# Performance work log

Measured on AMD Instinct MI355X. Metric: run time of the kernel, lower is better.

## Reference

```python
import jax, jax.numpy as jnp
import numpy as np

N_NODES = 50000
N_EDGES = 800000
D_IN, D_HID, D_OUT, D_EDGE = 128, 256, 128, 16


def setup_inputs() -> dict:
    key = jax.random.key(0)
    ks = jax.random.split(key, 6)
    nh = jax.random.normal(ks[0], (N_NODES, D_IN), dtype=jnp.float32)
    eh = jax.random.normal(ks[1], (N_EDGES, D_EDGE), dtype=jnp.float32)
    edge_index = jax.random.randint(ks[2], (2, N_EDGES), 0, N_NODES, dtype=jnp.int32)
    # MLP params (build_layer: Linear(d_in,d_hid) -> relu -> Linear(d_hid,d_out)), scaled init
    W1 = jax.random.normal(ks[3], (D_IN, D_HID), dtype=jnp.float32) / np.sqrt(D_IN)
    b1 = jnp.zeros((D_HID,), dtype=jnp.float32)
    W2 = jax.random.normal(ks[4], (D_HID, D_OUT), dtype=jnp.float32) / np.sqrt(D_HID)
    b2 = jnp.zeros((D_OUT,), dtype=jnp.float32)
    return {"nh": nh, "eh": eh, "edge_index": edge_index,
            "W1": W1, "b1": b1, "W2": W2, "b2": b2}


def reference(nh, eh, edge_index, W1, b1, W2, b2):
    n_nodes = nh.shape[0]
    # nf_lin: 2-layer MLP with relu
    n_h = jax.nn.relu(nh @ W1 + b1) @ W2 + b2          # [N, d]
    src, dst = edge_index[0], edge_index[1]
    src_nh = n_h[src]                                   # [E, d] gather
    dst_nh = n_h[dst]                                   # [E, d] gather
    attn = jnp.sum(src_nh * dst_nh, axis=-1)            # [E] per-edge score
    # segment softmax over edges grouped by destination node
    seg_max = jax.ops.segment_max(attn, dst, num_segments=n_nodes)  # [N]
    e = jnp.exp(attn - seg_max[dst])                    # [E] stable exp
    denom = jax.ops.segment_sum(e, dst, num_segments=n_nodes)       # [N]
    attn = e / denom[dst]                               # [E]
    # weighted scatter-add aggregation
    nz = jax.ops.segment_sum(attn[:, None] * src_nh, dst, num_segments=n_nodes)  # [N, d]
    return (n_h + nz, eh)
```

## Files before the change

kernel.cpp:

```cpp
#include <hip/hip_runtime.h>
#include <math.h>


#define D_IN   128
#define D_HID  256
#define D_OUT  128

typedef short bf16x8 __attribute__((ext_vector_type(8)));
typedef float f32x4  __attribute__((ext_vector_type(4)));

__device__ __forceinline__ short f2bf(float f)
{
    unsigned int u = __float_as_uint(f);
    unsigned int r = (u + 0x7fffu + ((u >> 16) & 1u)) >> 16;
    return (short)r;
}
__device__ __forceinline__ float bf2f(short h)
{
    return __uint_as_float(((unsigned int)(unsigned short)h) << 16);
}

__device__ __forceinline__ void pack_body(const float* __restrict__ W,
                                          short* __restrict__ Bh,
                                          short* __restrict__ Bl,
                                          int K, int N, int u)
{
    const int T = K >> 5;
    const int l = u & 63;
    const int t = (u >> 6) % T;
    const int c = u / (64 * T);
    const int lr = l & 15, kb = l >> 4;
    bf16x8 vh, vl;
#pragma unroll
    for (int j = 0; j < 8; ++j) {
        int k   = t * 32 + kb * 8 + j;
        int col = c * 16 + lr;
        float x = W[(size_t)k * N + col];
        short hi = f2bf(x);
        vh[j] = hi;
        vl[j] = f2bf(x - bf2f(hi));
    }
    *(bf16x8*)(Bh + (size_t)u * 8) = vh;
    *(bf16x8*)(Bl + (size_t)u * 8) = vl;
}

__global__ __launch_bounds__(256)
void prep(const float* __restrict__ A, short* __restrict__ Ah,
          short* __restrict__ Al, long valid, long total8, int nAB,
          const float* __restrict__ W1, short* __restrict__ B1h,
          short* __restrict__ B1l,
          const float* __restrict__ W2, short* __restrict__ B2h,
          short* __restrict__ B2l)
{
    int b = blockIdx.x;
    const int tid = threadIdx.x;
    if (b < nAB) {
        long t = (long)b * 256 + tid;
        if (t < total8) {
            long base = t * 8;
            bf16x8 vh, vl;
            if (base < valid) {
                float4 f0 = *(const float4*)(A + base);
                float4 f1 = *(const float4*)(A + base + 4);
                float fv[8] = {f0.x, f0.y, f0.z, f0.w, f1.x, f1.y, f1.z, f1.w};
#pragma unroll
                for (int j = 0; j < 8; ++j) {
                    short hi = f2bf(fv[j]);
                    vh[j] = hi;
                    vl[j] = f2bf(fv[j] - bf2f(hi));
                }
            } else {
                vh = (bf16x8)0; vl = (bf16x8)0;
            }
            *(bf16x8*)(Ah + base) = vh;
            *(bf16x8*)(Al + base) = vl;
        }
        return;
    }
    b -= nAB;
    if (b < 16) pack_body(W1, B1h, B1l, D_IN, D_HID, b * 256 + tid);
    else        pack_body(W2, B2h, B2l, D_HID, D_OUT, (b - 16) * 256 + tid);
}

__global__ __launch_bounds__(256)
void hist_pos(const int* __restrict__ dst, unsigned int* __restrict__ count,
              unsigned int* __restrict__ pos, int E)
{
    int e = blockIdx.x * blockDim.x + threadIdx.x;
    if (e < E) pos[e] = atomicAdd(count + dst[e], 1u);
}

__global__ __launch_bounds__(256)
void chunk_sums(const unsigned int* __restrict__ count,
                unsigned int* __restrict__ bsum, int n)
{
    __shared__ unsigned int lds[256];
    const int t = threadIdx.x;
    const int i = blockIdx.x * 256 + t;
    lds[t] = (i < n) ? count[i] : 0u;
    __syncthreads();
#pragma unroll
    for (int d = 128; d > 0; d >>= 1) {
        if (t < d) lds[t] += lds[t + d];
        __syncthreads();
    }
    if (t == 0) bsum[blockIdx.x] = lds[0];
}

__global__ __launch_bounds__(256)
void scan_sums(const unsigned int* __restrict__ bsum,
               unsigned int* __restrict__ boff, int nb)
{
    __shared__ unsigned int lds[256];
    const int t = threadIdx.x;
    unsigned int v = (t < nb) ? bsum[t] : 0u;
    lds[t] = v;
    __syncthreads();
#pragma unroll
    for (int d = 1; d < 256; d <<= 1) {
        unsigned int x = lds[t];
        unsigned int add = (t >= d) ? lds[t - d] : 0u;
        __syncthreads();
        lds[t] = x + add;
        __syncthreads();
    }
    if (t < nb) boff[t] = lds[t] - v;
}

__global__ __launch_bounds__(256)
void write_off(const unsigned int* __restrict__ count,
               const unsigned int* __restrict__ boff,
               unsigned int* __restrict__ off, int n)
{
    __shared__ unsigned int lds[256];
    const int t = threadIdx.x;
    const int i = blockIdx.x * 256 + t;
    unsigned int v = (i < n) ? count[i] : 0u;
    lds[t] = v;
    __syncthreads();
#pragma unroll
    for (int d = 1; d < 256; d <<= 1) {
        unsigned int x = lds[t];
        unsigned int add = (t >= d) ? lds[t - d] : 0u;
        __syncthreads();
        lds[t] = x + add;
        __syncthreads();
    }
    unsigned int incl = lds[t];
    unsigned int base = boff[blockIdx.x];
    if (i < n)  off[i] = base + incl - v;
    if (i == n - 1) off[n] = base + incl;
}

__global__ __launch_bounds__(256)
void fill_srcs(const int* __restrict__ src, const int* __restrict__ dst,
               const unsigned int* __restrict__ off,
               const unsigned int* __restrict__ pos,
               int* __restrict__ srcs, int E)
{
    int e = blockIdx.x * blockDim.x + threadIdx.x;
    if (e >= E) return;
    srcs[off[dst[e]] + pos[e]] = src[e];
}

#define H2_STRIDE 264

__global__ __launch_bounds__(256)
void mlp_fused(const short* __restrict__ Ah, const short* __restrict__ Al,
               const short* __restrict__ B1h, const short* __restrict__ B1l,
               const float* __restrict__ b1,
               const short* __restrict__ B2h, const short* __restrict__ B2l,
               const float* __restrict__ b2,
               float* __restrict__ out, short* __restrict__ nhb, int Nvalid)
{
    __shared__ __attribute__((aligned(16))) short H[64 * H2_STRIDE];

    const int w  = threadIdx.x >> 6;
    const int l  = threadIdx.x & 63;
    const int lr = l & 15, kb = l >> 4;
    const size_t row0 = (size_t)blockIdx.x * 64;

    f32x4 acc1[4][4] = {};
#pragma unroll
    for (int t = 0; t < 4; ++t) {
        bf16x8 ah[4], al[4], bh[4], bl[4];
#pragma unroll
        for (int m = 0; m < 4; ++m) {
            size_t aoff = (row0 + m * 16 + lr) * D_IN + t * 32 + kb * 8;
            ah[m] = *(const bf16x8*)(Ah + aoff);
            al[m] = *(const bf16x8*)(Al + aoff);
        }
#pragma unroll
        for (int n = 0; n < 4; ++n) {
            int c = w * 4 + n;
            size_t boff = (size_t)((c * 4 + t) * 64 + l) * 8;
            bh[n] = *(const bf16x8*)(B1h + boff);
            bl[n] = *(const bf16x8*)(B1l + boff);
        }
#pragma unroll
        for (int m = 0; m < 4; ++m)
#pragma unroll
            for (int n = 0; n < 4; ++n) {
                acc1[m][n] = __builtin_amdgcn_mfma_f32_16x16x32_bf16(ah[m], bh[n], acc1[m][n], 0, 0, 0);
                acc1[m][n] = __builtin_amdgcn_mfma_f32_16x16x32_bf16(al[m], bh[n], acc1[m][n], 0, 0, 0);
                acc1[m][n] = __builtin_amdgcn_mfma_f32_16x16x32_bf16(ah[m], bl[n], acc1[m][n], 0, 0, 0);
            }
    }

#pragma unroll
    for (int n = 0; n < 4; ++n) {
        int col = w * 64 + n * 16 + lr;
        float bb = b1[col];
#pragma unroll
        for (int m = 0; m < 4; ++m)
#pragma unroll
            for (int i = 0; i < 4; ++i) {
                int lrow = m * 16 + kb * 4 + i;
                float v = fmaxf(acc1[m][n][i] + bb, 0.f);
                H[lrow * H2_STRIDE + col] = f2bf(v);
            }
    }
    __syncthreads();

    f32x4 acc2[4][2] = {};
#pragma unroll
    for (int t2 = 0; t2 < 8; ++t2) {
        bf16x8 a[4], bh[2], bl[2];
#pragma unroll
        for (int m = 0; m < 4; ++m)
            a[m] = *(const bf16x8*)&H[(m * 16 + lr) * H2_STRIDE + t2 * 32 + kb * 8];
#pragma unroll
        for (int n = 0; n < 2; ++n) {
            int c = w * 2 + n;
            size_t boff = (size_t)((c * 8 + t2) * 64 + l) * 8;
            bh[n] = *(const bf16x8*)(B2h + boff);
            bl[n] = *(const bf16x8*)(B2l + boff);
        }
#pragma unroll
        for (int m = 0; m < 4; ++m)
#pragma unroll
            for (int n = 0; n < 2; ++n) {
                acc2[m][n] = __builtin_amdgcn_mfma_f32_16x16x32_bf16(a[m], bh[n], acc2[m][n], 0, 0, 0);
                acc2[m][n] = __builtin_amdgcn_mfma_f32_16x16x32_bf16(a[m], bl[n], acc2[m][n], 0, 0, 0);
            }
    }

#pragma unroll
    for (int n = 0; n < 2; ++n) {
        int col = w * 32 + n * 16 + lr;
        float bb = b2[col];
#pragma unroll
        for (int m = 0; m < 4; ++m)
#pragma unroll
            for (int i = 0; i < 4; ++i) {
                size_t row = row0 + m * 16 + kb * 4 + i;
                float v = acc2[m][n][i] + bb;
                nhb[row * D_OUT + col] = f2bf(v);
                if ((int)row < Nvalid) out[row * D_OUT + col] = v;
            }
    }
}

#define NEG_HUGE -3.0e38f

__global__ __launch_bounds__(256)
void agg_copy(const short* __restrict__ nhb,
              const unsigned int* __restrict__ off,
              const int* __restrict__ srcs,
              float* __restrict__ out, int N,
              const f32x4* __restrict__ ehin, f32x4* __restrict__ ehout,
              int n4, int copyB)
{
    if ((int)blockIdx.x < copyB) {
        for (int i = blockIdx.x * 256 + threadIdx.x; i < n4; i += copyB * 256) {
            f32x4 v = __builtin_nontemporal_load(ehin + i);
            __builtin_nontemporal_store(v, ehout + i);
        }
        return;
    }
    int wid  = (((int)blockIdx.x - copyB) * 256 + (int)threadIdx.x) >> 6;
    int lane = threadIdx.x & 63;
    if (wid >= N) return;
    const int g = lane >> 4;
    const int j = lane & 15;

    const float* sp = out + (size_t)wid * D_OUT + j * 8;
    const float4 sa = *(const float4*)sp;
    const float4 sb = *(const float4*)(sp + 4);

    const unsigned int beg = off[wid];
    const unsigned int end = off[wid + 1];

    float m = NEG_HUGE, den = 0.f;
    float c0 = 0.f, c1 = 0.f, c2 = 0.f, c3 = 0.f;
    float c4 = 0.f, c5 = 0.f, c6 = 0.f, c7 = 0.f;

    for (unsigned int base = beg; base < end; base += 8) {
        unsigned int idx0 = base + g * 2;
        unsigned int idx1 = idx0 + 1;
        bool v0 = idx0 < end, v1 = idx1 < end;
        int s0 = v0 ? srcs[idx0] : 0;
        int s1 = v1 ? srcs[idx1] : 0;
        uint4 A0 = *(const uint4*)(nhb + (size_t)s0 * D_OUT + j * 8);
        uint4 A1 = *(const uint4*)(nhb + (size_t)s1 * D_OUT + j * 8);

        float a00 = __uint_as_float(A0.x << 16), a01 = __uint_as_float(A0.x & 0xffff0000u);
        float a02 = __uint_as_float(A0.y << 16), a03 = __uint_as_float(A0.y & 0xffff0000u);
        float a04 = __uint_as_float(A0.z << 16), a05 = __uint_as_float(A0.z & 0xffff0000u);
        float a06 = __uint_as_float(A0.w << 16), a07 = __uint_as_float(A0.w & 0xffff0000u);
        float a10 = __uint_as_float(A1.x << 16), a11 = __uint_as_float(A1.x & 0xffff0000u);
        float a12 = __uint_as_float(A1.y << 16), a13 = __uint_as_float(A1.y & 0xffff0000u);
        float a14 = __uint_as_float(A1.z << 16), a15 = __uint_as_float(A1.z & 0xffff0000u);
        float a16 = __uint_as_float(A1.w << 16), a17 = __uint_as_float(A1.w & 0xffff0000u);

        float p0 = a00 * sa.x + a01 * sa.y + a02 * sa.z + a03 * sa.w
                 + a04 * sb.x + a05 * sb.y + a06 * sb.z + a07 * sb.w;
        float p1 = a10 * sa.x + a11 * sa.y + a12 * sa.z + a13 * sa.w
                 + a14 * sb.x + a15 * sb.y + a16 * sb.z + a17 * sb.w;
        p0 += __shfl_xor(p0, 1);  p1 += __shfl_xor(p1, 1);
        p0 += __shfl_xor(p0, 2);  p1 += __shfl_xor(p1, 2);
        p0 += __shfl_xor(p0, 4);  p1 += __shfl_xor(p1, 4);
        p0 += __shfl_xor(p0, 8);  p1 += __shfl_xor(p1, 8);

        float p0v = v0 ? p0 : NEG_HUGE;
        float p1v = v1 ? p1 : NEG_HUGE;
        float mnew = fmaxf(m, fmaxf(p0v, p1v));
        float scale = __expf(m - mnew);
        float w0 = v0 ? __expf(p0 - mnew) : 0.f;
        float w1 = v1 ? __expf(p1 - mnew) : 0.f;
        den = fmaf(den, scale, w0 + w1);
        c0 = fmaf(c0, scale, fmaf(w0, a00, w1 * a10));
        c1 = fmaf(c1, scale, fmaf(w0, a01, w1 * a11));
        c2 = fmaf(c2, scale, fmaf(w0, a02, w1 * a12));
        c3 = fmaf(c3, scale, fmaf(w0, a03, w1 * a13));
        c4 = fmaf(c4, scale, fmaf(w0, a04, w1 * a14));
        c5 = fmaf(c5, scale, fmaf(w0, a05, w1 * a15));
        c6 = fmaf(c6, scale, fmaf(w0, a06, w1 * a16));
        c7 = fmaf(c7, scale, fmaf(w0, a07, w1 * a17));
        m = mnew;
    }

    {
        float mg = m;
        m = fmaxf(m, __shfl_xor(m, 16));
        m = fmaxf(m, __shfl_xor(m, 32));
        float gs = __expf(mg - m);
        den *= gs;
        c0 *= gs; c1 *= gs; c2 *= gs; c3 *= gs;
        c4 *= gs; c5 *= gs; c6 *= gs; c7 *= gs;
#pragma unroll
        for (int o = 16; o < 64; o <<= 1) {
            den += __shfl_xor(den, o);
            c0 += __shfl_xor(c0, o); c1 += __shfl_xor(c1, o);
            c2 += __shfl_xor(c2, o); c3 += __shfl_xor(c3, o);
            c4 += __shfl_xor(c4, o); c5 += __shfl_xor(c5, o);
            c6 += __shfl_xor(c6, o); c7 += __shfl_xor(c7, o);
        }
    }

    float inv = (den > 0.f) ? 1.f / den : 0.f;
    if (g == 0) {
        float4 o0, o1;
        o0.x = sa.x + c0 * inv; o0.y = sa.y + c1 * inv;
        o0.z = sa.z + c2 * inv; o0.w = sa.w + c3 * inv;
        o1.x = sb.x + c4 * inv; o1.y = sb.y + c5 * inv;
        o1.z = sb.z + c6 * inv; o1.w = sb.w + c7 * inv;
        float* op = out + (size_t)wid * D_OUT + j * 8;
        *(float4*)op = o0;
        *(float4*)(op + 4) = o1;
    }
}

extern "C" void kernel_launch(void* const* d_in, const int* in_sizes, int n_in,
                              void* d_out, int out_size, void* d_ws, size_t ws_size,
                              hipStream_t stream)
{
    const float* nh  = (const float*)d_in[0];
    const float* eh  = (const float*)d_in[1];
    const int*   ei  = (const int*)d_in[2];
    const float* W1  = (const float*)d_in[3];
    const float* b1  = (const float*)d_in[4];
    const float* W2  = (const float*)d_in[5];
    const float* b2  = (const float*)d_in[6];

    const int N  = in_sizes[0] / D_IN;
    const int E  = in_sizes[2] / 2;
    const int EH = in_sizes[1];
    const int Mp = (N + 63) & ~63;
    const int NB = (N + 255) / 256;

    const int* src = ei;
    const int* dst = ei + E;

    float* out_nh = (float*)d_out;
    float* out_eh = (float*)d_out + (size_t)N * D_OUT;

    char* ws = (char*)d_ws;
    size_t o = 0;
    short* Ahp = (short*)(ws + o); o += (size_t)Mp * D_IN * 2;
    short* Alp = (short*)(ws + o); o += (size_t)Mp * D_IN * 2;
    short* nhb = (short*)(ws + o); o += (size_t)Mp * D_OUT * 2;
    short* B1h = (short*)(ws + o); o += (size_t)D_IN  * D_HID * 2;
    short* B1l = (short*)(ws + o); o += (size_t)D_IN  * D_HID * 2;
    short* B2h = (short*)(ws + o); o += (size_t)D_HID * D_OUT * 2;
    short* B2l = (short*)(ws + o); o += (size_t)D_HID * D_OUT * 2;
    int*          srcs  = (int*)(ws + o);          o += (size_t)E * 4;
    unsigned int* pos   = (unsigned int*)(ws + o); o += (size_t)E * 4;
    unsigned int* count = (unsigned int*)(ws + o); o += (size_t)N * 4;
    unsigned int* off   = (unsigned int*)(ws + o); o += (size_t)(N + 1) * 4;
    unsigned int* bsum  = (unsigned int*)(ws + o); o += (size_t)NB * 4;
    unsigned int* boff  = (unsigned int*)(ws + o); o += (size_t)NB * 4;

    (void)hipMemsetAsync(count, 0, (size_t)N * 4, stream);
    {
        long total8 = (long)Mp * D_IN / 8;
        int  nAB    = (int)((total8 + 255) / 256);
        prep<<<nAB + 32, 256, 0, stream>>>(
            nh, Ahp, Alp, (long)N * D_IN, total8, nAB,
            W1, B1h, B1l, W2, B2h, B2l);
    }

    hist_pos<<<(E + 255) / 256, 256, 0, stream>>>(dst, count, pos, E);
    chunk_sums<<<NB, 256, 0, stream>>>(count, bsum, N);
    scan_sums<<<1, 256, 0, stream>>>(bsum, boff, NB);
    write_off<<<NB, 256, 0, stream>>>(count, boff, off, N);
    fill_srcs<<<(E + 255) / 256, 256, 0, stream>>>(src, dst, off, pos, srcs, E);

    mlp_fused<<<Mp / 64, 256, 0, stream>>>(Ahp, Alp, B1h, B1l, b1,
                                           B2h, B2l, b2, out_nh, nhb, N);

    {
        int copyB = 512;
        int aggB  = (N + 3) / 4;
        agg_copy<<<copyB + aggB, 256, 0, stream>>>(
            nhb, off, srcs, out_nh, N,
            (const f32x4*)eh, (f32x4*)out_eh, EH / 4, copyB);
    }
}
```

Measured before the change: 161.1 us.

## Fuse CSR bucketing kernels into one cooperative kernel with grid syncs

Replaces the memset plus five separate bucketing kernels (histogram, chunk sums, scan, offsets, fill) with a single cooperative kernel of 1024 blocks that uses grid-wide syncs between phases. This removes several kernel launch gaps and the memset. In exchange each phase now runs with grid-stride loops over a fixed grid, and the scan phases keep only a few blocks busy while the others wait at barriers. Grid sync overhead and cooperative launch residency limits are added risks.

```diff
diff --git a/kernel.cpp b/kernel.cpp
--- a/kernel.cpp
+++ b/kernel.cpp
@@ -1,5 +1,8 @@
 #include <hip/hip_runtime.h>
+#include <hip/hip_cooperative_groups.h>
 #include <math.h>
+
+namespace cg = cooperative_groups;
 
 
 #define D_IN   128
@@ -83,84 +86,75 @@
 }
 
 __global__ __launch_bounds__(256)
-void hist_pos(const int* __restrict__ dst, unsigned int* __restrict__ count,
-              unsigned int* __restrict__ pos, int E)
-{
-    int e = blockIdx.x * blockDim.x + threadIdx.x;
-    if (e < E) pos[e] = atomicAdd(count + dst[e], 1u);
-}
-
-__global__ __launch_bounds__(256)
-void chunk_sums(const unsigned int* __restrict__ count,
-                unsigned int* __restrict__ bsum, int n)
-{
+void bucket_coop(const int* __restrict__ src, const int* __restrict__ dst,
+                 unsigned int* __restrict__ count, unsigned int* __restrict__ pos,
+                 unsigned int* __restrict__ off, unsigned int* __restrict__ bsum,
+                 unsigned int* __restrict__ boff, int* __restrict__ srcs,
+                 int N, int E, int NB)
+{
+    cg::grid_group grid = cg::this_grid();
     __shared__ unsigned int lds[256];
     const int t = threadIdx.x;
-    const int i = blockIdx.x * 256 + t;
-    lds[t] = (i < n) ? count[i] : 0u;
-    __syncthreads();
-#pragma unroll
-    for (int d = 128; d > 0; d >>= 1) {
-        if (t < d) lds[t] += lds[t + d];
+    const int b = blockIdx.x;
+    const int T = gridDim.x * 256;
+    const int gtid = b * 256 + t;
+
+    for (int i = gtid; i < N; i += T) count[i] = 0u;
+    grid.sync();
+
+    for (int e = gtid; e < E; e += T) pos[e] = atomicAdd(count + dst[e], 1u);
+    grid.sync();
+
+    if (b < NB) {
+        int i = b * 256 + t;
+        lds[t] = (i < N) ? count[i] : 0u;
         __syncthreads();
-    }
-    if (t == 0) bsum[blockIdx.x] = lds[0];
-}
-
-__global__ __launch_bounds__(256)
-void scan_sums(const unsigned int* __restrict__ bsum,
-               unsigned int* __restrict__ boff, int nb)
-{
-    __shared__ unsigned int lds[256];
-    const int t = threadIdx.x;
-    unsigned int v = (t < nb) ? bsum[t] : 0u;
-    lds[t] = v;
-    __syncthreads();
-#pragma unroll
-    for (int d = 1; d < 256; d <<= 1) {
-        unsigned int x = lds[t];
-        unsigned int add = (t >= d) ? lds[t - d] : 0u;
+#pragma unroll
+        for (int d = 128; d > 0; d >>= 1) {
+            if (t < d) lds[t] += lds[t + d];
+            __syncthreads();
+        }
+        if (t == 0) bsum[b] = lds[0];
+    }
+    grid.sync();
+
+    if (b == 0) {
+        unsigned int v = (t < NB) ? bsum[t] : 0u;
+        lds[t] = v;
         __syncthreads();
-        lds[t] = x + add;
+#pragma unroll
+        for (int d = 1; d < 256; d <<= 1) {
+            unsigned int x = lds[t];
+            unsigned int add = (t >= d) ? lds[t - d] : 0u;
+            __syncthreads();
+            lds[t] = x + add;
+            __syncthreads();
+        }
+        if (t < NB) boff[t] = lds[t] - v;
+    }
+    grid.sync();
+
+    if (b < NB) {
+        int i = b * 256 + t;
+        unsigned int v = (i < N) ? count[i] : 0u;
+        lds[t] = v;
         __syncthreads();
-    }
-    if (t < nb) boff[t] = lds[t] - v;
-}
-
-__global__ __launch_bounds__(256)
-void write_off(const unsigned int* __restrict__ count,
-               const unsigned int* __restrict__ boff,
-               unsigned int* __restrict__ off, int n)
-{
-    __shared__ unsigned int lds[256];
-    const int t = threadIdx.x;
-    const int i = blockIdx.x * 256 + t;
-    unsigned int v = (i < n) ? count[i] : 0u;
-    lds[t] = v;
-    __syncthreads();
-#pragma unroll
-    for (int d = 1; d < 256; d <<= 1) {
-        unsigned int x = lds[t];
-        unsigned int add = (t >= d) ? lds[t - d] : 0u;
-        __syncthreads();
-        lds[t] = x + add;
-        __syncthreads();
-    }
-    unsigned int incl = lds[t];
-    unsigned int base = boff[blockIdx.x];
-    if (i < n)  off[i] = base + incl - v;
-    if (i == n - 1) off[n] = base + incl;
-}
-
-__global__ __launch_bounds__(256)
-void fill_srcs(const int* __restrict__ src, const int* __restrict__ dst,
-               const unsigned int* __restrict__ off,
-               const unsigned int* __restrict__ pos,
-               int* __restrict__ srcs, int E)
-{
-    int e = blockIdx.x * blockDim.x + threadIdx.x;
-    if (e >= E) return;
-    srcs[off[dst[e]] + pos[e]] = src[e];
+#pragma unroll
+        for (int d = 1; d < 256; d <<= 1) {
+            unsigned int x = lds[t];
+            unsigned int add = (t >= d) ? lds[t - d] : 0u;
+            __syncthreads();
+            lds[t] = x + add;
+            __syncthreads();
+        }
+        unsigned int incl = lds[t];
+        unsigned int base = boff[b];
+        if (i < N)      off[i] = base + incl - v;
+        if (i == N - 1) off[N] = base + incl;
+    }
+    grid.sync();
+
+    for (int e = gtid; e < E; e += T) srcs[off[dst[e]] + pos[e]] = src[e];
 }
 
 #define H2_STRIDE 264
@@ -411,7 +405,6 @@
     unsigned int* bsum  = (unsigned int*)(ws + o); o += (size_t)NB * 4;
     unsigned int* boff  = (unsigned int*)(ws + o); o += (size_t)NB * 4;
 
-    (void)hipMemsetAsync(count, 0, (size_t)N * 4, stream);
     {
         long total8 = (long)Mp * D_IN / 8;
         int  nAB    = (int)((total8 + 255) / 256);
@@ -420,11 +413,17 @@
             W1, B1h, B1l, W2, B2h, B2l);
     }
 
-    hist_pos<<<(E + 255) / 256, 256, 0, stream>>>(dst, count, pos, E);
-    chunk_sums<<<NB, 256, 0, stream>>>(count, bsum, N);
-    scan_sums<<<1, 256, 0, stream>>>(bsum, boff, NB);
-    write_off<<<NB, 256, 0, stream>>>(count, boff, off, N);
-    fill_srcs<<<(E + 255) / 256, 256, 0, stream>>>(src, dst, off, pos, srcs, E);
+    {
+        int Nl = N, El = E, NBl = NB;
+        const int* srcl = src; const int* dstl = dst;
+        unsigned int* countl = count; unsigned int* posl = pos;
+        unsigned int* offl = off; unsigned int* bsuml = bsum;
+        unsigned int* boffl = boff; int* srcsl = srcs;
+        void* args[] = { &srcl, &dstl, &countl, &posl, &offl, &bsuml, &boffl,
+                         &srcsl, &Nl, &El, &NBl };
+        (void)hipLaunchCooperativeKernel((void*)bucket_coop, dim3(1024),
+                                         dim3(256), args, 0, stream);
+    }
 
     mlp_fused<<<Mp / 64, 256, 0, stream>>>(Ahp, Alp, B1h, B1l, b1,
                                            B2h, B2l, b2, out_nh, nhb, N);
```

Result: slower. 636.8 us (+295.2%).
